# Optimization experiments

Measured on AMD Instinct MI355X. Metric: run time of the kernel, lower is better.

The kernel has to match this reference:

```python
import jax, jax.numpy as jnp
import numpy as np

B, S1, S2 = 8, 2048, 2048
K1_DIM = K2_DIM = 512
PK1_DIM = PK2_DIM = 256
ATT_DIM = 512
DV = 512


def setup_inputs() -> dict:
    key = jax.random.key(0)
    ks = jax.random.split(key, 16)
    s = 0.02
    inp = {
        "k1": jax.random.normal(ks[0], (B, S1, K1_DIM), jnp.float32),
        "k2": jax.random.normal(ks[1], (B, S2, K2_DIM), jnp.float32),
        "preserved_k1": jax.random.normal(ks[2], (B, S1, PK1_DIM), jnp.float32),
        "preserved_k2": jax.random.normal(ks[3], (B, S2, PK2_DIM), jnp.float32),
        "v1": jax.random.normal(ks[4], (B, S1, DV), jnp.float32),
        "v2": jax.random.normal(ks[5], (B, S2, DV), jnp.float32),
        # Linear params stored as [in, out] (x @ W + b == torch Linear)
        "W_k1": jax.random.normal(ks[6], (K1_DIM, ATT_DIM), jnp.float32) * s,
        "b_k1": jnp.zeros((ATT_DIM,), jnp.float32),
        "W_k2": jax.random.normal(ks[7], (K2_DIM, ATT_DIM), jnp.float32) * s,
        "b_k2": jnp.zeros((ATT_DIM,), jnp.float32),
        "W_pk1": jax.random.normal(ks[8], (K1_DIM + PK1_DIM, ATT_DIM), jnp.float32) * s,
        "b_pk1": jnp.zeros((ATT_DIM,), jnp.float32),
        "W_pk2": jax.random.normal(ks[9], (K2_DIM + PK2_DIM, ATT_DIM), jnp.float32) * s,
        "b_pk2": jnp.zeros((ATT_DIM,), jnp.float32),
        # lengths in [S/2, S) so no softmax row is fully masked (original exits on NaN)
        "k1_lengths": jax.random.randint(ks[10], (B,), S1 // 2, S1, jnp.int32).astype(jnp.int64),
        "k2_lengths": jax.random.randint(ks[11], (B,), S2 // 2, S2, jnp.int32).astype(jnp.int64),
    }
    return inp


def _mask(k1_lengths, k2_lengths):
    # Faithful to the original loop: a position is masked iff EXACTLY ONE of
    # (row >= l1) / (col >= l2) holds (mask counter == 1, not >= 1).
    row_over = (jnp.arange(S1)[None, :, None] >= k1_lengths[:, None, None])  # [B,S1,1]
    col_over = (jnp.arange(S2)[None, None, :] >= k2_lengths[:, None, None])  # [B,1,S2]
    return (row_over.astype(jnp.int32) + col_over.astype(jnp.int32)) == 1  # [B,S1,S2]


def reference(k1, k2, preserved_k1, preserved_k2, v1, v2,
              W_k1, b_k1, W_k2, b_k2, W_pk1, b_pk1, W_pk2, b_pk2,
              k1_lengths, k2_lengths):
    pk1 = jnp.concatenate([k1, preserved_k1], axis=-1) @ W_pk1 + b_pk1  # [B,S1,A]
    pk2 = jnp.concatenate([k2, preserved_k2], axis=-1) @ W_pk2 + b_pk2  # [B,S2,A]
    k1p = k1 @ W_k1 + b_k1  # [B,S1,A]
    k2p = k2 @ W_k2 + b_k2  # [B,S2,A]

    score_1 = jnp.einsum("bsa,bta->bst", k1p, pk2)   # [B,S1,S2]
    score_2 = jnp.einsum("bsa,bta->bst", pk1, k2p)   # [B,S1,S2]

    mask = _mask(k1_lengths, k2_lengths)
    score_1 = jnp.where(mask, -jnp.inf, score_1)
    score_2 = jnp.where(mask, -jnp.inf, score_2)

    w1 = jax.nn.softmax(jnp.swapaxes(score_1, 1, 2), axis=-1)  # [B,S2,S1]
    w2 = jax.nn.softmax(score_2, axis=-1)                      # [B,S1,S2]

    o1 = jnp.einsum("bts,bsd->btd", w1, v1)  # [B,S2,DV]
    o2 = jnp.einsum("bst,btd->bsd", w2, v2)  # [B,S1,DV]
    # NOTE: original returns ragged per-sample slices of w1/w2; we return the
    # full padded weight matrices (slice w1[i,:l2,:l1], w2[i,:l1,:l2] to match).
    return (o1, o2, w1, w2)
```

## Files before the change

kernel.cpp:

```cpp
#include <hip/hip_runtime.h>

typedef _Float16 half8 __attribute__((ext_vector_type(8)));
typedef float    floatx4 __attribute__((ext_vector_type(4)));
typedef unsigned short u16;

constexpr int Bn  = 8;
constexpr int Sq  = 2048;
constexpr int KD  = 512;
constexpr int PKD = 256;
constexpr int AD  = 512;
constexpr int DV  = 512;

__device__ __forceinline__ void llds16(const void* g, void* l)
{
    __builtin_amdgcn_global_load_lds(
        (const __attribute__((address_space(1))) unsigned int*)g,
        (__attribute__((address_space(3))) unsigned int*)l, 16, 0, 0);
}

__global__ __launch_bounds__(256)
void transpose_cast_k(const float* __restrict__ in, _Float16* __restrict__ out,
                      int inRows, int inCols, long long bsIn, long long bsOut)
{
    __shared__ float t[32][33];
    const int b = blockIdx.z;
    in  += (long long)b * bsIn;
    out += (long long)b * bsOut;
    const int tx = threadIdx.x & 31;
    const int ty = threadIdx.x >> 5;
    const int c0 = blockIdx.x * 32;
    const int r0 = blockIdx.y * 32;
#pragma unroll
    for (int i = 0; i < 4; ++i)
        t[ty + 8*i][tx] = in[(long long)(r0 + ty + 8*i) * inCols + c0 + tx];
    __syncthreads();
#pragma unroll
    for (int i = 0; i < 4; ++i)
        out[(long long)(c0 + ty + 8*i) * inRows + r0 + tx] = (_Float16)t[tx][ty + 8*i];
}

template<bool A_F32, bool OUT_F16>
__global__ __launch_bounds__(256, 2)
void gemm_k(const void* __restrict__ A1v, const void* __restrict__ A2v, int Ksplit,
            int lda1, int lda2, long long bsA,
            const _Float16* __restrict__ Bm, int ldb, long long bsB,
            void* __restrict__ Cv, int ldc, long long bsC,
            const float* __restrict__ bias, int K)
{
    __shared__ __align__(16) unsigned char AsRaw[A_F32 ? 16384 : 8192];
    __shared__ __align__(16) unsigned char BsRaw[8192];

    const int tid  = threadIdx.x;
    const int lane = tid & 63;
    const int wave = tid >> 6;
    const int wm   = (wave >> 1) * 64;
    const int wn   = (wave & 1) * 64;
    const int fr   = lane & 15;
    const int fq   = lane >> 4;

    const int tm = blockIdx.y, tn = blockIdx.x, bz = blockIdx.z;
    const long long aRowBase = (long long)tm * 128;
    const long long bRowBase = (long long)tn * 128;
    const _Float16* Bbase = Bm + (long long)bz * bsB;

    floatx4 acc[4][4];
#pragma unroll
    for (int i = 0; i < 4; ++i)
#pragma unroll
        for (int j = 0; j < 4; ++j) acc[i][j] = (floatx4)0.0f;

    for (int k0 = 0; k0 < K; k0 += 32) {
        __syncthreads();

        if (A_F32) {
            const float* A1 = (const float*)A1v + (long long)bz * bsA;
            const float* A2 = (const float*)A2v;
#pragma unroll
            for (int is = 0; is < 4; ++is) {
                const int r  = (tid >> 3) + is * 32;
                const int ch = (tid & 7) ^ (r & 7);
                const int kk = k0 + ch * 4;
                const float* src = (kk < Ksplit)
                    ? A1 + (aRowBase + r) * lda1 + kk
                    : A2 + (aRowBase + r) * lda2 + (kk - Ksplit);
                llds16(src, AsRaw + tid * 16 + is * 4096);
            }
        } else {
            const _Float16* A1 = (const _Float16*)A1v + (long long)bz * bsA;
#pragma unroll
            for (int is = 0; is < 2; ++is) {
                const int r  = (tid >> 2) + is * 64;
                const int ch = (tid & 3) ^ (r & 3);
                llds16(A1 + (aRowBase + r) * lda1 + k0 + ch * 8,
                       AsRaw + tid * 16 + is * 4096);
            }
        }
#pragma unroll
        for (int is = 0; is < 2; ++is) {
            const int r  = (tid >> 2) + is * 64;
            const int ch = (tid & 3) ^ (r & 3);
            llds16(Bbase + (bRowBase + r) * ldb + k0 + ch * 8,
                   BsRaw + tid * 16 + is * 4096);
        }

        __syncthreads();

        half8 af[4], bf[4];
        if (A_F32) {
            const float* As32 = (const float*)AsRaw;
#pragma unroll
            for (int i = 0; i < 4; ++i) {
                const int r  = wm + i * 16 + fr;
                const int c0 = ((2 * fq) ^ (r & 7)) * 4;
                const int c1 = ((2 * fq + 1) ^ (r & 7)) * 4;
                floatx4 f0 = *(const floatx4*)(As32 + r * 32 + c0);
                floatx4 f1 = *(const floatx4*)(As32 + r * 32 + c1);
                half8 h;
#pragma unroll
                for (int j = 0; j < 4; ++j) {
                    h[j]     = (_Float16)f0[j];
                    h[4 + j] = (_Float16)f1[j];
                }
                af[i] = h;
            }
        } else {
            const _Float16* As16 = (const _Float16*)AsRaw;
#pragma unroll
            for (int i = 0; i < 4; ++i) {
                const int r  = wm + i * 16 + fr;
                const int ch = fq ^ (r & 3);
                af[i] = *(const half8*)(As16 + r * 32 + ch * 8);
            }
        }
        {
            const _Float16* Bs16 = (const _Float16*)BsRaw;
#pragma unroll
            for (int j = 0; j < 4; ++j) {
                const int r  = wn + j * 16 + fr;
                const int ch = fq ^ (r & 3);
                bf[j] = *(const half8*)(Bs16 + r * 32 + ch * 8);
            }
        }
#pragma unroll
        for (int i = 0; i < 4; ++i)
#pragma unroll
            for (int j = 0; j < 4; ++j)
                acc[i][j] = __builtin_amdgcn_mfma_f32_16x16x32_f16(af[i], bf[j], acc[i][j], 0, 0, 0);
    }

    const int crow0 = tm * 128 + wm + fq * 4;
    const int ccol0 = tn * 128 + wn + fr;
    if (OUT_F16) {
        _Float16* C = (_Float16*)Cv + (long long)bz * bsC;
#pragma unroll
        for (int i = 0; i < 4; ++i)
#pragma unroll
            for (int j = 0; j < 4; ++j) {
                const int col = ccol0 + j * 16;
                const float bv = bias[col];
#pragma unroll
                for (int r = 0; r < 4; ++r)
                    C[(long long)(crow0 + i*16 + r) * ldc + col] = (_Float16)(acc[i][j][r] + bv);
            }
    } else {
        float* C = (float*)Cv + (long long)bz * bsC;
#pragma unroll
        for (int i = 0; i < 4; ++i)
#pragma unroll
            for (int j = 0; j < 4; ++j) {
                const int col = ccol0 + j * 16;
#pragma unroll
                for (int r = 0; r < 4; ++r)
                    C[(long long)(crow0 + i*16 + r) * ldc + col] = acc[i][j][r];
            }
    }
}

__device__ __forceinline__ int load_len(const int* __restrict__ p, int b)
{
    return (p[1] == 0) ? p[2 * b] : p[b];
}

__global__ __launch_bounds__(256)
void softmax_mask_k(float* __restrict__ w, _Float16* __restrict__ wh,
                    const int* __restrict__ lenR, const int* __restrict__ lenC)
{
    const int b = blockIdx.y;
    const int r = blockIdx.x;
    const long long rowOff = ((long long)b * Sq + r) * (long long)Sq;
    float* row = w + rowOff;
    const int lr = load_len(lenR, b);
    const int lc = load_len(lenC, b);
    const bool rover = (r >= lr);
    const int tid  = threadIdx.x;
    const int lane = tid & 63;
    const int wave = tid >> 6;

    floatx4 x0 = *(const floatx4*)(row + tid * 8);
    floatx4 x1 = *(const floatx4*)(row + tid * 8 + 4);
    float v[8];
#pragma unroll
    for (int j = 0; j < 4; ++j) { v[j] = x0[j]; v[4 + j] = x1[j]; }

    float m = -3.0e38f;
#pragma unroll
    for (int j = 0; j < 8; ++j) {
        const int c = tid * 8 + j;
        if (rover != (c >= lc)) v[j] = -__builtin_inff();
        m = fmaxf(m, v[j]);
    }
#pragma unroll
    for (int off = 32; off > 0; off >>= 1) m = fmaxf(m, __shfl_xor(m, off, 64));
    __shared__ float redm[4], reds[4];
    if (lane == 0) redm[wave] = m;
    __syncthreads();
    m = fmaxf(fmaxf(redm[0], redm[1]), fmaxf(redm[2], redm[3]));

    float s = 0.f;
#pragma unroll
    for (int j = 0; j < 8; ++j) { v[j] = __expf(v[j] - m); s += v[j]; }
#pragma unroll
    for (int off = 32; off > 0; off >>= 1) s += __shfl_xor(s, off, 64);
    if (lane == 0) reds[wave] = s;
    __syncthreads();
    s = reds[0] + reds[1] + reds[2] + reds[3];
    const float inv = 1.0f / s;
#pragma unroll
    for (int j = 0; j < 4; ++j) { x0[j] = v[j] * inv; x1[j] = v[4 + j] * inv; }
    *(floatx4*)(row + tid * 8)     = x0;
    *(floatx4*)(row + tid * 8 + 4) = x1;
    if (wh != nullptr) {
        half8 h;
#pragma unroll
        for (int j = 0; j < 4; ++j) { h[j] = (_Float16)x0[j]; h[4 + j] = (_Float16)x1[j]; }
        *(half8*)(wh + rowOff + tid * 8) = h;
    }
}

extern "C" void kernel_launch(void* const* d_in, const int* in_sizes, int n_in,
                              void* d_out, int out_size, void* d_ws, size_t ws_size,
                              hipStream_t stream)
{
    (void)in_sizes; (void)n_in; (void)out_size;
    const float* k1    = (const float*)d_in[0];
    const float* k2    = (const float*)d_in[1];
    const float* pk1in = (const float*)d_in[2];
    const float* pk2in = (const float*)d_in[3];
    const float* v1    = (const float*)d_in[4];
    const float* v2    = (const float*)d_in[5];
    const float* W_k1  = (const float*)d_in[6];
    const float* b_k1  = (const float*)d_in[7];
    const float* W_k2  = (const float*)d_in[8];
    const float* b_k2  = (const float*)d_in[9];
    const float* W_pk1 = (const float*)d_in[10];
    const float* b_pk1 = (const float*)d_in[11];
    const float* W_pk2 = (const float*)d_in[12];
    const float* b_pk2 = (const float*)d_in[13];
    const int* len1 = (const int*)d_in[14];
    const int* len2 = (const int*)d_in[15];

    float* out = (float*)d_out;
    float* o1 = out;
    float* o2 = o1 + (long long)Bn * Sq * DV;
    float* w1 = o2 + (long long)Bn * Sq * DV;
    float* w2 = w1 + (long long)Bn * Sq * Sq;

    _Float16* k1p = (_Float16*)o1;
    _Float16* k2p = k1p + (long long)Bn * Sq * AD;
    _Float16* pk1 = (_Float16*)o2;
    _Float16* pk2 = pk1 + (long long)Bn * Sq * AD;

    _Float16* vT1   = (_Float16*)d_ws;
    _Float16* vT2   = vT1 + (long long)Bn * DV * Sq;
    _Float16* WTk1  = vT2 + (long long)Bn * DV * Sq;
    _Float16* WTk2  = WTk1 + AD * KD;
    _Float16* WTpk1 = WTk2 + AD * KD;
    _Float16* WTpk2 = WTpk1 + AD * (KD + PKD);

    const unsigned long long fixedHalves =
        2ull * Bn * DV * Sq + 2ull * AD * KD + 2ull * AD * (KD + PKD);
    _Float16* w1h = (_Float16*)d_ws + fixedHalves;
    _Float16* w2h = w1h + (long long)Bn * Sq * Sq;
    const bool fast =
        ws_size >= (fixedHalves + 2ull * Bn * Sq * Sq) * sizeof(_Float16);

    transpose_cast_k<<<dim3(AD/32, KD/32, 1), 256, 0, stream>>>(W_k1, WTk1, KD, AD, 0, 0);
    transpose_cast_k<<<dim3(AD/32, KD/32, 1), 256, 0, stream>>>(W_k2, WTk2, KD, AD, 0, 0);
    transpose_cast_k<<<dim3(AD/32, (KD+PKD)/32, 1), 256, 0, stream>>>(W_pk1, WTpk1, KD+PKD, AD, 0, 0);
    transpose_cast_k<<<dim3(AD/32, (KD+PKD)/32, 1), 256, 0, stream>>>(W_pk2, WTpk2, KD+PKD, AD, 0, 0);
    transpose_cast_k<<<dim3(DV/32, Sq/32, Bn), 256, 0, stream>>>(v1, vT1, Sq, DV,
        (long long)Sq*DV, (long long)Sq*DV);
    transpose_cast_k<<<dim3(DV/32, Sq/32, Bn), 256, 0, stream>>>(v2, vT2, Sq, DV,
        (long long)Sq*DV, (long long)Sq*DV);

    const dim3 gProj(AD/128, (Bn*Sq)/128, 1);
    gemm_k<true, true><<<gProj, 256, 0, stream>>>(
        k1, k1, KD, KD, KD, 0,  WTk1, KD, 0,  k1p, AD, 0, b_k1, KD);
    gemm_k<true, true><<<gProj, 256, 0, stream>>>(
        k2, k2, KD, KD, KD, 0,  WTk2, KD, 0,  k2p, AD, 0, b_k2, KD);
    gemm_k<true, true><<<gProj, 256, 0, stream>>>(
        k1, pk1in, KD, KD, PKD, 0,  WTpk1, KD+PKD, 0,  pk1, AD, 0, b_pk1, KD+PKD);
    gemm_k<true, true><<<gProj, 256, 0, stream>>>(
        k2, pk2in, KD, KD, PKD, 0,  WTpk2, KD+PKD, 0,  pk2, AD, 0, b_pk2, KD+PKD);

    const dim3 gScore(Sq/128, Sq/128, Bn);
    gemm_k<false, false><<<gScore, 256, 0, stream>>>(
        pk2, pk2, 0, AD, AD, (long long)Sq*AD,
        k1p, AD, (long long)Sq*AD,
        w1, Sq, (long long)Sq*Sq, nullptr, AD);
    gemm_k<false, false><<<gScore, 256, 0, stream>>>(
        pk1, pk1, 0, AD, AD, (long long)Sq*AD,
        k2p, AD, (long long)Sq*AD,
        w2, Sq, (long long)Sq*Sq, nullptr, AD);

    softmax_mask_k<<<dim3(Sq, Bn), 256, 0, stream>>>(w1, fast ? w1h : nullptr, len2, len1);
    softmax_mask_k<<<dim3(Sq, Bn), 256, 0, stream>>>(w2, fast ? w2h : nullptr, len1, len2);

    const dim3 gOut(DV/128, Sq/128, Bn);
    if (fast) {
        gemm_k<false, false><<<gOut, 256, 0, stream>>>(
            w1h, w1h, 0, Sq, Sq, (long long)Sq*Sq,
            vT1, Sq, (long long)DV*Sq,
            o1, DV, (long long)Sq*DV, nullptr, Sq);
        gemm_k<false, false><<<gOut, 256, 0, stream>>>(
            w2h, w2h, 0, Sq, Sq, (long long)Sq*Sq,
            vT2, Sq, (long long)DV*Sq,
            o2, DV, (long long)Sq*DV, nullptr, Sq);
    } else {
        gemm_k<true, false><<<gOut, 256, 0, stream>>>(
            w1, w1, Sq, Sq, Sq, (long long)Sq*Sq,
            vT1, Sq, (long long)DV*Sq,
            o1, DV, (long long)Sq*DV, nullptr, Sq);
        gemm_k<true, false><<<gOut, 256, 0, stream>>>(
            w2, w2, Sq, Sq, Sq, (long long)Sq*Sq,
            vT2, Sq, (long long)DV*Sq,
            o2, DV, (long long)Sq*DV, nullptr, Sq);
    }
}
```

Measured before the change: 932.6 us.

## Add 256x256-tile double-buffered MFMA GEMM for the score matmuls

Adds a dedicated score GEMM kernel that uses 256x256 output tiles with 512 threads. It double-buffers swizzled LDS tiles filled by direct global-to-LDS loads, splits each K step into four quadrant phases with barriers and raised wave priority around the MFMAs, and remaps block indices for L2 locality. The larger tiles raise arithmetic intensity and overlap loading with compute for the two S×S score products. The cost is 128KB of LDS and heavy register pressure per block, which limits occupancy.

```diff
diff --git a/kernel.cpp b/kernel.cpp
--- a/kernel.cpp
+++ b/kernel.cpp
@@ -174,6 +174,139 @@
                     C[(long long)(crow0 + i*16 + r) * ldc + col] = acc[i][j][r];
             }
     }
+}
+
+__global__ __launch_bounds__(512, 2)
+void gemm256_k(const _Float16* __restrict__ Am, long long bsA, int lda,
+               const _Float16* __restrict__ Bm, long long bsB, int ldb,
+               float* __restrict__ Cm, long long bsC, int ldc, int K)
+{
+    __shared__ __align__(16) _Float16 lds[65536];
+
+    const int lin0 = (blockIdx.z * 8 + blockIdx.y) * 8 + blockIdx.x;
+    const int lin  = (lin0 & 7) * 64 + (lin0 >> 3);
+    const int tn   = lin & 7;
+    const int tm   = (lin >> 3) & 7;
+    const int bz   = lin >> 6;
+
+    const int tid  = threadIdx.x;
+    const int lane = tid & 63;
+    const int wave = tid >> 6;
+    const int wm   = (wave >> 2) * 128;
+    const int wn   = (wave & 3) * 64;
+    const int fr   = lane & 15;
+    const int fq   = lane >> 4;
+
+    const _Float16* Ab = Am + (long long)bz * bsA + (long long)tm * 256 * lda;
+    const _Float16* Bb = Bm + (long long)bz * bsB + (long long)tn * 256 * ldb;
+
+    const int sr = lane >> 3;
+    const int ch = (lane & 7) ^ sr;
+    const _Float16* srcA[2][2];
+    const _Float16* srcB[2][2];
+#pragma unroll
+    for (int h = 0; h < 2; ++h)
+#pragma unroll
+        for (int l = 0; l < 2; ++l) {
+            const int r = h * 128 + (wave * 2 + l) * 8 + sr;
+            srcA[h][l] = Ab + (long long)r * lda + ch * 8;
+            srcB[h][l] = Bb + (long long)r * ldb + ch * 8;
+        }
+
+    auto stageA = [&](int kt, int buf) {
+#pragma unroll
+        for (int h = 0; h < 2; ++h)
+#pragma unroll
+            for (int l = 0; l < 2; ++l)
+                llds16(srcA[h][l] + kt * 64,
+                       lds + buf * 32768 + h * 8192 + (wave * 2 + l) * 512 + lane * 8);
+    };
+    auto stageB = [&](int kt, int buf) {
+#pragma unroll
+        for (int h = 0; h < 2; ++h)
+#pragma unroll
+            for (int l = 0; l < 2; ++l)
+                llds16(srcB[h][l] + kt * 64,
+                       lds + buf * 32768 + 16384 + h * 8192 + (wave * 2 + l) * 512 + lane * 8);
+    };
+
+    auto rdA = [&](int buf, int im, int kk) -> half8 {
+        const int row = wm + im * 16 + fr;
+        const int c   = (kk * 4 + fq) ^ (row & 7);
+        return *(const half8*)(lds + buf * 32768 + row * 64 + c * 8);
+    };
+    auto rdB = [&](int buf, int jn, int kk) -> half8 {
+        const int row = wn + jn * 16 + fr;
+        const int c   = (kk * 4 + fq) ^ (row & 7);
+        return *(const half8*)(lds + buf * 32768 + 16384 + row * 64 + c * 8);
+    };
+
+    floatx4 acc[8][4];
+#pragma unroll
+    for (int i = 0; i < 8; ++i)
+#pragma unroll
+        for (int j = 0; j < 4; ++j) acc[i][j] = (floatx4)0.0f;
+
+    const int KT = K >> 6;
+
+    stageA(0, 0);
+    stageB(0, 0);
+    __syncthreads();
+
+    for (int kt = 0; kt < KT; ++kt) {
+        const int buf = kt & 1;
+        half8 af[4][2], bf[2][2];
+#pragma unroll
+        for (int q = 0; q < 4; ++q) {
+            const int nh = q >> 1;
+            const int mh = (q == 1 || q == 2) ? 1 : 0;
+            if (q == 0 || q == 2) {
+#pragma unroll
+                for (int j = 0; j < 2; ++j)
+#pragma unroll
+                    for (int kk = 0; kk < 2; ++kk)
+                        bf[j][kk] = rdB(buf, nh * 2 + j, kk);
+            }
+            if (q != 2) {
+#pragma unroll
+                for (int i = 0; i < 4; ++i)
+#pragma unroll
+                    for (int kk = 0; kk < 2; ++kk)
+                        af[i][kk] = rdA(buf, mh * 4 + i, kk);
+            }
+            if (kt + 1 < KT) {
+                if (q == 0)      stageA(kt + 1, buf ^ 1);
+                else if (q == 1) stageB(kt + 1, buf ^ 1);
+            }
+            __builtin_amdgcn_s_barrier();
+            __builtin_amdgcn_s_setprio(1);
+#pragma unroll
+            for (int i = 0; i < 4; ++i)
+#pragma unroll
+                for (int j = 0; j < 2; ++j)
+#pragma unroll
+                    for (int kk = 0; kk < 2; ++kk)
+                        acc[mh * 4 + i][nh * 2 + j] =
+                            __builtin_amdgcn_mfma_f32_16x16x32_f16(
+                                af[i][kk], bf[j][kk], acc[mh * 4 + i][nh * 2 + j], 0, 0, 0);
+            __builtin_amdgcn_s_setprio(0);
+            if (q < 3) __builtin_amdgcn_s_barrier();
+        }
+        __syncthreads();
+    }
+
+    float* Cb = Cm + (long long)bz * bsC;
+    const int crow0 = tm * 256 + wm + fq * 4;
+    const int ccol0 = tn * 256 + wn + fr;
+#pragma unroll
+    for (int i = 0; i < 8; ++i)
+#pragma unroll
+        for (int j = 0; j < 4; ++j) {
+            const long long base = (long long)(crow0 + i * 16) * ldc + ccol0 + j * 16;
+#pragma unroll
+            for (int r = 0; r < 4; ++r)
+                Cb[base + (long long)r * ldc] = acc[i][j][r];
+        }
 }
 
 __device__ __forceinline__ int load_len(const int* __restrict__ p, int b)
@@ -303,15 +436,15 @@
     gemm_k<true, true><<<gProj, 256, 0, stream>>>(
         k2, pk2in, KD, KD, PKD, 0,  WTpk2, KD+PKD, 0,  pk2, AD, 0, b_pk2, KD+PKD);
 
-    const dim3 gScore(Sq/128, Sq/128, Bn);
-    gemm_k<false, false><<<gScore, 256, 0, stream>>>(
-        pk2, pk2, 0, AD, AD, (long long)Sq*AD,
-        k1p, AD, (long long)Sq*AD,
-        w1, Sq, (long long)Sq*Sq, nullptr, AD);
-    gemm_k<false, false><<<gScore, 256, 0, stream>>>(
-        pk1, pk1, 0, AD, AD, (long long)Sq*AD,
-        k2p, AD, (long long)Sq*AD,
-        w2, Sq, (long long)Sq*Sq, nullptr, AD);
+    const dim3 gScore(Sq/256, Sq/256, Bn);
+    gemm256_k<<<gScore, 512, 0, stream>>>(
+        pk2, (long long)Sq*AD, AD,
+        k1p, (long long)Sq*AD, AD,
+        w1, (long long)Sq*Sq, Sq, AD);
+    gemm256_k<<<gScore, 512, 0, stream>>>(
+        pk1, (long long)Sq*AD, AD,
+        k2p, (long long)Sq*AD, AD,
+        w2, (long long)Sq*Sq, Sq, AD);
 
     softmax_mask_k<<<dim3(Sq, Bn), 256, 0, stream>>>(w1, fast ? w1h : nullptr, len2, len1);
     softmax_mask_k<<<dim3(Sq, Bn), 256, 0, stream>>>(w2, fast ? w2h : nullptr, len1, len2);
```

New measurement: 906.1 us. -2.8%, faster.
